# Kernel optimization log

Hardware: AMD Instinct MI355X
Metric: run time of the kernel (lower is better)

## Reference

```python
import jax, jax.numpy as jnp
import numpy as np

F_, OF, OW, L, H, NH = 40, 8, 24, 3, 128, 4
G = F_ // OF  # 5 groups
B, T = 32, 512


def setup_inputs() -> dict:
    key = jax.random.key(0)
    ks = jax.random.split(key, 17)
    s = 0.08
    rn = lambda k, shape: jax.random.normal(k, shape, jnp.float32) * s
    return {
        "x": jax.random.normal(ks[0], (B, F_, T), jnp.float32),
        # per-feature stacked 3-layer LSTM params (PyTorch gate order i,f,g,o)
        "w_ih0": rn(ks[1], (F_, 4 * H, 1)),
        "w_ih12": rn(ks[2], (L - 1, F_, 4 * H, H)),
        "w_hh": rn(ks[3], (L, F_, 4 * H, H)),
        "b_ih": rn(ks[4], (L, F_, 4 * H)),
        "b_hh": rn(ks[5], (L, F_, 4 * H)),
        # per-group MHA params
        "g_wqkv": rn(ks[6], (G, 3 * H, H)),
        "g_bqkv": rn(ks[7], (G, 3 * H)),
        "g_wo": rn(ks[8], (G, H, H)),
        "g_bo": rn(ks[9], (G, H)),
        # final MHA params
        "f_wqkv": rn(ks[10], (3 * H, H)),
        "f_bqkv": rn(ks[11], (3 * H,)),
        "f_wo": rn(ks[12], (H, H)),
        "f_bo": rn(ks[13], (H,)),
        # output FC
        "fc_w": rn(ks[14], (OF * OW, H)),
        "fc_b": rn(ks[15], (OF * OW,)),
    }


def _lstm_layer(xw, whh, bhh):
    # xw: [F,B,T,4H] precomputed input projections; scan over time
    h0 = jnp.zeros(xw.shape[:2] + (H,), xw.dtype)
    def step(carry, xt):
        h, c = carry
        gates = xt + jnp.einsum('fbh,fgh->fbg', h, whh) + bhh[:, None, :]
        i, f, g, o = jnp.split(gates, 4, axis=-1)
        c = jax.nn.sigmoid(f) * c + jax.nn.sigmoid(i) * jnp.tanh(g)
        h = jax.nn.sigmoid(o) * jnp.tanh(c)
        return (h, c), h
    (hT, _), hs = jax.lax.scan(step, (h0, h0), jnp.moveaxis(xw, 2, 0))
    return jnp.moveaxis(hs, 0, 2), hT  # seq [F,B,T,H], last [F,B,H]


def _mha(q, k, v, wqkv, bqkv, wo, bo):
    wq, wk, wv = jnp.split(wqkv, 3, axis=0)
    bq, bk, bv = jnp.split(bqkv, 3, axis=0)
    hd = H // NH
    def proj(t, w, b):
        p = t @ w.T + b
        return p.reshape(t.shape[:-1] + (NH, hd)).swapaxes(-3, -2)  # [..,NH,S,hd]
    qh, kh, vh = proj(q, wq, bq), proj(k, wk, bk), proj(v, wv, bv)
    scores = jnp.einsum('bnqd,bnkd->bnqk', qh, kh) / np.float32(np.sqrt(hd))
    attn = jax.nn.softmax(scores, axis=-1)
    out = jnp.einsum('bnqk,bnkd->bnqd', attn, vh).swapaxes(-3, -2).reshape(q.shape)
    return out @ wo.T + bo


def reference(x, w_ih0, w_ih12, w_hh, b_ih, b_hh, g_wqkv, g_bqkv, g_wo, g_bo,
              f_wqkv, f_bqkv, f_wo, f_bo, fc_w, fc_b):
    bsz = x.shape[0]
    h_seq = jnp.transpose(x, (1, 0, 2))[..., None]  # [F,B,T,1]
    h_last = None
    for l in range(L):  # 3 stacked LSTM layers, all 40 feature-LSTMs batched
        wih = w_ih0 if l == 0 else w_ih12[l - 1]
        xw = jnp.einsum('fbti,fgi->fbtg', h_seq, wih) + b_ih[l][:, None, None, :]
        h_seq, h_last = _lstm_layer(xw, w_hh[l], b_hh[l])
    features = jnp.transpose(h_last, (1, 0, 2))  # [B,F,H]
    groups = features.reshape(bsz, G, OF, H).swapaxes(0, 1)  # [G,B,OF,H]
    gattn = jax.vmap(lambda g, w, b, wo, bo: _mha(g, g, g, w, b, wo, bo))(
        groups, g_wqkv, g_bqkv, g_wo, g_bo)  # [G,B,OF,H]
    pooled = gattn.mean(axis=2).swapaxes(0, 1)  # [B,G,H]
    fin = _mha(pooled, pooled, pooled, f_wqkv, f_bqkv, f_wo, f_bo)  # [B,G,H]
    emb = fin[:, 0, :]  # target_coin_index = 0
    return (emb @ fc_w.T + fc_b).reshape(bsz, OF, OW)
```

## Files before the change

### kernel.cpp

```cpp
#include <hip/hip_runtime.h>
#include <cstdint>
#include <cstddef>


#define NFEAT 40
#define TDIM  512

typedef __bf16 bf16x8 __attribute__((ext_vector_type(8)));
typedef float floatx4 __attribute__((ext_vector_type(4)));
typedef float floatx2 __attribute__((ext_vector_type(2)));
typedef int   intx4   __attribute__((ext_vector_type(4)));
typedef unsigned short u16;

#if __has_builtin(__builtin_amdgcn_exp2f)
#define EXP2F __builtin_amdgcn_exp2f
#else
#define EXP2F exp2f
#endif
#if __has_builtin(__builtin_amdgcn_rcpf)
#define RCPF __builtin_amdgcn_rcpf
#else
#define RCPF(x) (1.f / (x))
#endif

#define MF(a, b, c) __builtin_amdgcn_mfma_f32_16x16x32_bf16( \
    __builtin_bit_cast(bf16x8, (a)), __builtin_bit_cast(bf16x8, (b)), (c), 0, 0, 0)

#define NEG_LOG2E -1.44269504f

__device__ __forceinline__ float bf2f(u16 s) {
  union { unsigned u; float f; } v; v.u = ((unsigned)s) << 16; return v.f;
}
__device__ __forceinline__ unsigned f2bf(float f) {
  union { float f; unsigned u; } v; v.f = f;
  unsigned u = v.u + 0x7fffu + ((v.u >> 16) & 1u);
  return (u >> 16);
}

#define RING_FSTRIDE 1048576
#define RING_TSTRIDE 4096
#define RING_MASK    255

__global__ void prep_kernel(const float* __restrict__ w_ih12,
                            const float* __restrict__ w_hh,
                            const float* __restrict__ b_ih,
                            const float* __restrict__ b_hh,
                            u16* __restrict__ Whh,
                            u16* __restrict__ Wih,
                            float* __restrict__ biasAll,
                            int* __restrict__ flags)
{
  const int N_hh4 = 3 * NFEAT * 512 * 128 / 4;
  const int N_ih4 = 2 * NFEAT * 512 * 128 / 4;
  const int NB    = 3 * NFEAT * 512;
  const int NF    = 384;
  const int total = N_hh4 + N_ih4 + NB + NF;
  for (int idx = blockIdx.x * blockDim.x + threadIdx.x; idx < total;
       idx += gridDim.x * blockDim.x) {
    if (idx < N_hh4 + N_ih4) {
      const bool ih = (idx >= N_hh4);
      const int i4 = (ih ? idx - N_hh4 : idx) * 4;
      const float4 v = *(const float4*)((ih ? w_ih12 : w_hh) + i4);
      uint2 p;
      p.x = (f2bf(v.y * NEG_LOG2E) << 16) | f2bf(v.x * NEG_LOG2E);
      p.y = (f2bf(v.w * NEG_LOG2E) << 16) | f2bf(v.z * NEG_LOG2E);
      *(uint2*)((ih ? Wih : Whh) + i4) = p;
    } else if (idx < N_hh4 + N_ih4 + NB) {
      int i = idx - N_hh4 - N_ih4;
      biasAll[i] = (b_ih[i] + b_hh[i]) * NEG_LOG2E;
    } else {
      flags[idx - N_hh4 - N_ih4 - NB] = 0;
    }
  }
}

template <int LAYER>
__device__ __forceinline__ void lstm_body(
    const u16* __restrict__ Wh, const u16* __restrict__ Wx,
    const float* __restrict__ bias,
    const float* __restrict__ xin, const float* __restrict__ w0,
    const u16* __restrict__ ringIn, u16* __restrict__ ringOut,
    u16* __restrict__ hlast,
    int* __restrict__ flagIn,
    int* __restrict__ flagOut,
    int* __restrict__ flagConsIn,
    int* __restrict__ flagConsOut,
    int f, int half, u16* __restrict__ Abase)
{
  constexpr bool IS_L0   = (LAYER == 0);
  constexpr bool IS_LAST = (LAYER == 2);

  const int tid  = threadIdx.x;
  const int wave = tid >> 6;
  const int lane = tid & 63;
  const int m15  = lane & 15;
  const int q    = lane >> 4;
  const int kb   = q * 8;
  const int wq4  = wave * 16 + q * 4;

#define ALDS(P, M, K) (Abase + ((P) * 16 + (M)) * 136 + (K))

  intx4 whf[4][4];
  const size_t wbase = (size_t)f * 512 * 128;
#pragma unroll
  for (int g = 0; g < 4; ++g)
#pragma unroll
    for (int kt = 0; kt < 4; ++kt)
      whf[g][kt] = *(const intx4*)(Wh + wbase +
          (size_t)(g * 128 + wave * 16 + m15) * 128 + kt * 32 + kb);

  intx4 wxf[4][4];
  if constexpr (!IS_L0) {
#pragma unroll
    for (int g = 0; g < 4; ++g)
#pragma unroll
      for (int kt = 0; kt < 4; ++kt)
        wxf[g][kt] = *(const intx4*)(Wx + wbase +
            (size_t)(g * 128 + wave * 16 + m15) * 128 + kt * 32 + kb);
  }

  floatx4 bv[4], w0v[4];
#pragma unroll
  for (int g = 0; g < 4; ++g) {
    bv[g] = *(const floatx4*)(bias + f * 512 + g * 128 + wq4);
    if constexpr (IS_L0) {
      floatx4 wv = *(const floatx4*)(w0 + f * 512 + g * 128 + wq4);
      w0v[g] = wv * NEG_LOG2E;
    }
  }

  for (int idx = tid; idx < 2 * 16 * 136; idx += 512) Abase[idx] = 0;

  if constexpr (LAYER >= 1) {
    if (tid == 0) {
      while (__hip_atomic_load(flagIn, __ATOMIC_RELAXED,
                               __HIP_MEMORY_SCOPE_AGENT) < 19)
        __builtin_amdgcn_s_sleep(2);
      __threadfence();
    }
  }
  __syncthreads();

  const u16* xbase = (LAYER >= 1)
      ? ringIn + (size_t)f * RING_FSTRIDE + (half * 16 + m15) * 128 + kb
      : nullptr;
  const float* xsbase = IS_L0
      ? xin + ((size_t)(half * 16 + m15) * NFEAT + f) * 512
      : nullptr;

  floatx4 accx0[4], accx1[4];
  intx4 xf0[4], xf1[4];
  float xsc[2] = {0.f, 0.f};

  if constexpr (!IS_L0) {
    intx4 p0[4];
#pragma unroll
    for (int kt = 0; kt < 4; ++kt) p0[kt]  = *(const intx4*)(xbase + kt * 32);
#pragma unroll
    for (int kt = 0; kt < 4; ++kt)
      xf0[kt] = *(const intx4*)(xbase + 1 * RING_TSTRIDE + kt * 32);
#pragma unroll
    for (int kt = 0; kt < 4; ++kt)
      xf1[kt] = *(const intx4*)(xbase + 2 * RING_TSTRIDE + kt * 32);
#pragma unroll
    for (int g = 0; g < 4; ++g) {
      floatx4 a = bv[g];
#pragma unroll
      for (int kt = 0; kt < 4; ++kt) a = MF(wxf[g][kt], p0[kt], a);
      accx0[g] = a;
    }
  } else {
    const float x0 = xsbase[0];
    xsc[0] = xsbase[1];
    xsc[1] = xsbase[2];
#pragma unroll
    for (int g = 0; g < 4; ++g) accx0[g] = bv[g] + w0v[g] * x0;
  }

  float creg[4] = {0.f, 0.f, 0.f, 0.f};
  u16* hb_ring = (LAYER <= 1)
      ? ringOut + (size_t)f * RING_FSTRIDE + (half * 16 + m15) * 128 + wq4
      : nullptr;
  uint2 hdef;

#define LSTM_STEP(PC, ACC_C, ACC_N, XF_C, T)                                   \
  {                                                                            \
                                            \
    if (((T) & 15) == 0 && (T) > 0) {                                          \
      if (tid == 0) {                                                          \
        if constexpr (LAYER >= 1) {                                            \
          int tgt = (T) + 19; if (tgt > 512) tgt = 512;                        \
          while (__hip_atomic_load(flagIn, __ATOMIC_RELAXED,                   \
                                   __HIP_MEMORY_SCOPE_AGENT) < tgt)            \
            __builtin_amdgcn_s_sleep(2);                                       \
        }                                                                      \
        if constexpr (LAYER <= 1) {                                            \
                               \
          while (__hip_atomic_load(flagConsIn, __ATOMIC_RELAXED,               \
                                   __HIP_MEMORY_SCOPE_AGENT) < (T) - 290)      \
            __builtin_amdgcn_s_sleep(2);                                       \
        }                                                                      \
        __threadfence();       \
        if constexpr (LAYER <= 1)                                              \
          __hip_atomic_store(flagOut, (T) - 2, __ATOMIC_RELAXED,               \
                             __HIP_MEMORY_SCOPE_AGENT);                        \
        if constexpr (LAYER >= 1)                                              \
          __hip_atomic_store(flagConsOut, (T), __ATOMIC_RELAXED,               \
                             __HIP_MEMORY_SCOPE_AGENT);                        \
      }                                                                        \
      if constexpr (LAYER >= 1) __syncthreads();                               \
    }                                                                          \
                                 \
    if constexpr (!IS_LAST) {                                                  \
      if ((T) > 0)                                                             \
        *(uint2*)(hb_ring + (size_t)(((T) - 1) & RING_MASK) * RING_TSTRIDE) =  \
            hdef;                                                              \
    }                                                                          \
                                            \
    intx4 xn0, xn1, xn2, xn3;                                                  \
    float xns = 0.f;                                                           \
    {                                                                          \
      const int tl = ((T) + 3 < TDIM) ? (T) + 3 : TDIM - 1;                    \
      if constexpr (!IS_L0) {                                                  \
        const u16* xp = xbase + (size_t)(tl & RING_MASK) * RING_TSTRIDE;       \
        xn0 = *(const intx4*)(xp);                                             \
        xn1 = *(const intx4*)(xp + 32);                                        \
        xn2 = *(const intx4*)(xp + 64);                                        \
        xn3 = *(const intx4*)(xp + 96);                                        \
      } else {                                                                 \
        xns = xsbase[tl];                                                      \
      }                                                                        \
    }                                                                          \
                                                     \
    intx4 hf0 = *(const intx4*)ALDS(PC, m15, kb);                              \
    intx4 hf1 = *(const intx4*)ALDS(PC, m15, 32 + kb);                         \
    intx4 hf2 = *(const intx4*)ALDS(PC, m15, 64 + kb);                         \
    intx4 hf3 = *(const intx4*)ALDS(PC, m15, 96 + kb);                         \
                                                   \
    floatx4 ac0 = MF(whf[0][0], hf0, ACC_C[0]);                                \
    floatx4 ac1 = MF(whf[1][0], hf0, ACC_C[1]);                                \
    floatx4 ac2 = MF(whf[2][0], hf0, ACC_C[2]);                                \
    floatx4 ac3 = MF(whf[3][0], hf0, ACC_C[3]);                                \
    ac0 = MF(whf[0][1], hf1, ac0); ac1 = MF(whf[1][1], hf1, ac1);              \
    ac2 = MF(whf[2][1], hf1, ac2); ac3 = MF(whf[3][1], hf1, ac3);              \
    ac0 = MF(whf[0][2], hf2, ac0); ac1 = MF(whf[1][2], hf2, ac1);              \
    ac2 = MF(whf[2][2], hf2, ac2); ac3 = MF(whf[3][2], hf2, ac3);              \
    ac0 = MF(whf[0][3], hf3, ac0); ac1 = MF(whf[1][3], hf3, ac1);              \
    ac2 = MF(whf[2][3], hf3, ac2); ac3 = MF(whf[3][3], hf3, ac3);              \
             \
    if constexpr (!IS_L0) {                                                    \
      floatx4 n0 = bv[0], n1 = bv[1], n2 = bv[2], n3 = bv[3];                  \
      n0 = MF(wxf[0][0], XF_C[0], n0); n1 = MF(wxf[1][0], XF_C[0], n1);        \
      n2 = MF(wxf[2][0], XF_C[0], n2); n3 = MF(wxf[3][0], XF_C[0], n3);        \
      n0 = MF(wxf[0][1], XF_C[1], n0); n1 = MF(wxf[1][1], XF_C[1], n1);        \
      n2 = MF(wxf[2][1], XF_C[1], n2); n3 = MF(wxf[3][1], XF_C[1], n3);        \
      n0 = MF(wxf[0][2], XF_C[2], n0); n1 = MF(wxf[1][2], XF_C[2], n1);        \
      n2 = MF(wxf[2][2], XF_C[2], n2); n3 = MF(wxf[3][2], XF_C[2], n3);        \
      n0 = MF(wxf[0][3], XF_C[3], n0); n1 = MF(wxf[1][3], XF_C[3], n1);        \
      n2 = MF(wxf[2][3], XF_C[3], n2); n3 = MF(wxf[3][3], XF_C[3], n3);        \
      ACC_N[0] = n0; ACC_N[1] = n1; ACC_N[2] = n2; ACC_N[3] = n3;              \
      XF_C[0] = xn0; XF_C[1] = xn1; XF_C[2] = xn2; XF_C[3] = xn3;              \
    } else {                                                                   \
      const float xn = xsc[PC];                                                \
      ACC_N[0] = bv[0] + w0v[0] * xn; ACC_N[1] = bv[1] + w0v[1] * xn;          \
      ACC_N[2] = bv[2] + w0v[2] * xn; ACC_N[3] = bv[3] + w0v[3] * xn;          \
      xsc[PC] = xns;                                                           \
    }                                                                          \
                 \
    unsigned hlo, hhi;                                                         \
    {                                                                          \
      float hv[4];                                                             \
      _Pragma("unroll")                                                        \
      for (int r = 0; r < 4; ++r) {                                            \
        const float Ei = EXP2F(ac0[r]);                                        \
        const float Ef = EXP2F(ac1[r]);                                        \
        const float Eg = EXP2F(2.f * ac2[r]);                                  \
        const float Eo = EXP2F(ac3[r]);                                        \
        const float Pp = (1.f + Ei) * (1.f + Eg);                              \
        const float Qq = 1.f + Ef;                                             \
        const float c  = (creg[r] * Pp + Qq * (1.f - Eg)) * RCPF(Qq * Pp);     \
        creg[r] = c;                                                           \
        const float Ec = EXP2F(-2.88539008f * c);                              \
        hv[r] = (1.f - Ec) * RCPF((1.f + Ec) * (1.f + Eo));                    \
      }                                                                        \
      hlo = (f2bf(hv[1]) << 16) | f2bf(hv[0]);                                 \
      hhi = (f2bf(hv[3]) << 16) | f2bf(hv[2]);                                 \
    }                                                                          \
    uint2 hp; hp.x = hlo; hp.y = hhi;                                          \
    *(uint2*)ALDS((PC) ^ 1, m15, wq4) = hp;                                    \
    hdef = hp;                                                                 \
    __syncthreads();                                                           \
  }

#pragma unroll 1
  for (int t = 0; t < TDIM; t += 2) {
    LSTM_STEP(0, accx0, accx1, xf0, t);
    LSTM_STEP(1, accx1, accx0, xf1, t + 1);
  }
#undef LSTM_STEP
#undef ALDS

  if constexpr (!IS_LAST) {
    *(uint2*)(hb_ring + (size_t)(511 & RING_MASK) * RING_TSTRIDE) = hdef;
    __syncthreads();
    if (tid == 0) {
      __threadfence();
      __hip_atomic_store(flagOut, 512, __ATOMIC_RELAXED,
                         __HIP_MEMORY_SCOPE_AGENT);
    }
  } else {
    *(uint2*)(hlast + ((size_t)f * 32 + half * 16 + m15) * 128 + wq4) = hdef;
  }
}

__global__ __launch_bounds__(512, 2) void lstm_fused(
    const u16* __restrict__ Whh, const u16* __restrict__ Wih,
    const float* __restrict__ biasAll,
    const float* __restrict__ xin, const float* __restrict__ w0,
    u16* __restrict__ ring0, u16* __restrict__ ring1,
    u16* __restrict__ hlast, int* __restrict__ flags)
{
  __shared__ __align__(16) u16 A[2 * 16 * 136];
  const int layer = blockIdx.x / 80;
  const int bx    = blockIdx.x % 80;
  const int f = bx >> 1, half = bx & 1;
  const size_t LSL = (size_t)NFEAT * 512 * 128;

  if (layer == 0) {
    lstm_body<0>(Whh, nullptr, biasAll, xin, w0,
                 nullptr, ring0, nullptr,
                 nullptr, flags + bx, flags + 160 + bx, nullptr,
                 f, half, A);
  } else if (layer == 1) {
    lstm_body<1>(Whh + LSL, Wih, biasAll + NFEAT * 512, nullptr, nullptr,
                 ring0, ring1, nullptr,
                 flags + bx, flags + 80 + bx, flags + 240 + bx,
                 flags + 160 + bx, f, half, A);
  } else {
    lstm_body<2>(Whh + 2 * LSL, Wih + LSL, biasAll + 2 * NFEAT * 512,
                 nullptr, nullptr, ring1, nullptr, hlast,
                 flags + 80 + bx, nullptr, nullptr, flags + 240 + bx,
                 f, half, A);
  }
}

__global__ void gattn_kernel(const u16* __restrict__ hlast,
                             const float* __restrict__ g_wqkv,
                             const float* __restrict__ g_bqkv,
                             const float* __restrict__ g_wo,
                             const float* __restrict__ g_bo,
                             float* __restrict__ pooled)
{
  const int tid = threadIdx.x;
  const int g = blockIdx.x >> 5;
  const int b = blockIdx.x & 31;

  __shared__ float feat[8][128];
  __shared__ float qkv[8][384];
  __shared__ float sc[4][8][8];
  __shared__ float colsum[4][8];
  __shared__ float poolin[128];

  for (int idx = tid; idx < 8 * 128; idx += 128) {
    int of = idx >> 7, j = idx & 127;
    int f = g * 8 + of;
    feat[of][j] = bf2f(hlast[((size_t)f * 32 + b) * 128 + j]);
  }
  __syncthreads();
  for (int idx = tid; idx < 8 * 384; idx += 128) {
    int of = idx / 384, r = idx - of * 384;
    const float* wr = g_wqkv + ((size_t)g * 384 + r) * 128;
    float s = 0.f;
    for (int j = 0; j < 128; ++j) s += feat[of][j] * wr[j];
    qkv[of][r] = s + g_bqkv[g * 384 + r];
  }
  __syncthreads();
  for (int idx = tid; idx < 256; idx += 128) {
    int n = idx >> 6, qp = (idx >> 3) & 7, kp = idx & 7;
    float s = 0.f;
    for (int d = 0; d < 32; ++d)
      s += qkv[qp][n * 32 + d] * qkv[kp][128 + n * 32 + d];
    sc[n][qp][kp] = s * 0.17677669529663687f;
  }
  __syncthreads();
  if (tid < 32) {
    int n = tid >> 3, qp = tid & 7;
    float mx = -1e30f;
    for (int kp = 0; kp < 8; ++kp) mx = fmaxf(mx, sc[n][qp][kp]);
    float e[8], sum = 0.f;
    for (int kp = 0; kp < 8; ++kp) { e[kp] = __expf(sc[n][qp][kp] - mx); sum += e[kp]; }
    float inv = 1.f / sum;
    for (int kp = 0; kp < 8; ++kp) sc[n][qp][kp] = e[kp] * inv;
  }
  __syncthreads();
  if (tid < 32) {
    int n = tid >> 3, kp = tid & 7;
    float s = 0.f;
    for (int qp = 0; qp < 8; ++qp) s += sc[n][qp][kp];
    colsum[n][kp] = s;
  }
  __syncthreads();
  {
    int n = tid >> 5;
    float s = 0.f;
    for (int kp = 0; kp < 8; ++kp) s += colsum[n][kp] * qkv[kp][256 + tid];
    poolin[tid] = s;
  }
  __syncthreads();
  {
    const float* wr = g_wo + ((size_t)g * 128 + tid) * 128;
    float s = 0.f;
    for (int i = 0; i < 128; ++i) s += poolin[i] * wr[i];
    pooled[((size_t)b * 5 + g) * 128 + tid] = s * 0.125f + g_bo[g * 128 + tid];
  }
}

__global__ void final_kernel(const float* __restrict__ pooled,
                             const float* __restrict__ f_wqkv,
                             const float* __restrict__ f_bqkv,
                             const float* __restrict__ f_wo,
                             const float* __restrict__ f_bo,
                             const float* __restrict__ fc_w,
                             const float* __restrict__ fc_b,
                             float* __restrict__ out)
{
  const int tid = threadIdx.x;
  const int b = blockIdx.x;

  __shared__ float P[5][128];
  __shared__ float q0[128];
  __shared__ float kbuf[5][128];
  __shared__ float vbuf[5][128];
  __shared__ float attn[4][5];
  __shared__ float ao[128];
  __shared__ float fin[128];

  for (int idx = tid; idx < 640; idx += 192) {
    int g = idx >> 7, j = idx & 127;
    P[g][j] = pooled[((size_t)b * 5 + g) * 128 + j];
  }
  __syncthreads();
  for (int idx = tid; idx < 1408; idx += 192) {
    int kind, pos, r;
    if (idx < 128)       { kind = 0; pos = 0;                 r = idx; }
    else if (idx < 768)  { kind = 1; pos = (idx - 128) >> 7;  r = (idx - 128) & 127; }
    else                 { kind = 2; pos = (idx - 768) >> 7;  r = (idx - 768) & 127; }
    const int wrow = kind * 128 + r;
    const float* wr = f_wqkv + (size_t)wrow * 128;
    const float* src = P[kind == 0 ? 0 : pos];
    float s = 0.f;
    for (int j = 0; j < 128; ++j) s += src[j] * wr[j];
    s += f_bqkv[wrow];
    if (kind == 0) q0[r] = s;
    else if (kind == 1) kbuf[pos][r] = s;
    else vbuf[pos][r] = s;
  }
  __syncthreads();
  if (tid < 20) {
    int n = tid / 5, kp = tid - n * 5;
    float s = 0.f;
    for (int d = 0; d < 32; ++d) s += q0[n * 32 + d] * kbuf[kp][n * 32 + d];
    attn[n][kp] = s * 0.17677669529663687f;
  }
  __syncthreads();
  if (tid < 4) {
    float mx = -1e30f;
    for (int kp = 0; kp < 5; ++kp) mx = fmaxf(mx, attn[tid][kp]);
    float sum = 0.f;
    for (int kp = 0; kp < 5; ++kp) { float e = __expf(attn[tid][kp] - mx); attn[tid][kp] = e; sum += e; }
    float inv = 1.f / sum;
    for (int kp = 0; kp < 5; ++kp) attn[tid][kp] *= inv;
  }
  __syncthreads();
  if (tid < 128) {
    int n = tid >> 5;
    float s = 0.f;
    for (int kp = 0; kp < 5; ++kp) s += attn[n][kp] * vbuf[kp][tid];
    ao[tid] = s;
  }
  __syncthreads();
  if (tid < 128) {
    const float* wr = f_wo + (size_t)tid * 128;
    float s = 0.f;
    for (int i = 0; i < 128; ++i) s += ao[i] * wr[i];
    fin[tid] = s + f_bo[tid];
  }
  __syncthreads();
  {
    const float* wr = fc_w + (size_t)tid * 128;
    float s = 0.f;
    for (int j = 0; j < 128; ++j) s += fin[j] * wr[j];
    out[(size_t)b * 192 + tid] = s + fc_b[tid];
  }
}

extern "C" void kernel_launch(void* const* d_in, const int* in_sizes, int n_in,
                              void* d_out, int out_size, void* d_ws, size_t ws_size,
                              hipStream_t stream)
{
  const float* x      = (const float*)d_in[0];
  const float* w_ih0  = (const float*)d_in[1];
  const float* w_ih12 = (const float*)d_in[2];
  const float* w_hh   = (const float*)d_in[3];
  const float* b_ih   = (const float*)d_in[4];
  const float* b_hh   = (const float*)d_in[5];
  const float* g_wqkv = (const float*)d_in[6];
  const float* g_bqkv = (const float*)d_in[7];
  const float* g_wo   = (const float*)d_in[8];
  const float* g_bo   = (const float*)d_in[9];
  const float* f_wqkv = (const float*)d_in[10];
  const float* f_bqkv = (const float*)d_in[11];
  const float* f_wo   = (const float*)d_in[12];
  const float* f_bo   = (const float*)d_in[13];
  const float* fc_w   = (const float*)d_in[14];
  const float* fc_b   = (const float*)d_in[15];

  const size_t N_hh = (size_t)3 * NFEAT * 512 * 128;
  const size_t N_ih = (size_t)2 * NFEAT * 512 * 128;
  const size_t NB   = (size_t)3 * NFEAT * 512;
  const size_t RSZ  = (size_t)NFEAT * 256 * 4096;

  u16* Whh       = (u16*)d_ws;
  u16* Wih       = Whh + N_hh;
  float* biasAll = (float*)(Wih + N_ih);
  u16* ring0     = (u16*)(biasAll + NB);
  u16* ring1     = ring0 + RSZ;
  u16* hlast     = ring1 + RSZ;
  int* flags     = (int*)(hlast + (size_t)NFEAT * 32 * 128);
  float* pooled  = (float*)(flags + 384);

  prep_kernel<<<4096, 256, 0, stream>>>(w_ih12, w_hh, b_ih, b_hh,
                                        Whh, Wih, biasAll, flags);

  lstm_fused<<<240, 512, 0, stream>>>(Whh, Wih, biasAll, x, w_ih0,
                                      ring0, ring1, hlast, flags);

  gattn_kernel<<<160, 128, 0, stream>>>(hlast, g_wqkv, g_bqkv, g_wo, g_bo, pooled);
  final_kernel<<<32, 192, 0, stream>>>(pooled, f_wqkv, f_bqkv, f_wo, f_bo,
                                       fc_w, fc_b, (float*)d_out);
}
```

Before: 977.8 us.

## Replace threadfence with agent-scope atomic ring accesses and tighten consumer lag

```diff
diff --git a/kernel.cpp b/kernel.cpp
--- a/kernel.cpp
+++ b/kernel.cpp
@@ -8,9 +8,9 @@
 
 typedef __bf16 bf16x8 __attribute__((ext_vector_type(8)));
 typedef float floatx4 __attribute__((ext_vector_type(4)));
-typedef float floatx2 __attribute__((ext_vector_type(2)));
 typedef int   intx4   __attribute__((ext_vector_type(4)));
 typedef unsigned short u16;
+typedef unsigned long long u64;
 
 #if __has_builtin(__builtin_amdgcn_exp2f)
 #define EXP2F __builtin_amdgcn_exp2f
@@ -35,6 +35,19 @@
   union { float f; unsigned u; } v; v.f = f;
   unsigned u = v.u + 0x7fffu + ((v.u >> 16) & 1u);
   return (u >> 16);
+}
+
+__device__ __forceinline__ void st_ring8(u16* p, uint2 v) {
+  u64 q = ((u64)v.y << 32) | (u64)v.x;
+  __hip_atomic_store((u64*)p, q, __ATOMIC_RELAXED, __HIP_MEMORY_SCOPE_AGENT);
+}
+__device__ __forceinline__ intx4 ld_ring16(const u16* p) {
+  union { u64 q[2]; intx4 v; } u;
+  u.q[0] = __hip_atomic_load((const u64*)p, __ATOMIC_RELAXED,
+                             __HIP_MEMORY_SCOPE_AGENT);
+  u.q[1] = __hip_atomic_load((const u64*)(p + 4), __ATOMIC_RELAXED,
+                             __HIP_MEMORY_SCOPE_AGENT);
+  return u.v;
 }
 
 #define RING_FSTRIDE 1048576
@@ -136,7 +149,6 @@
       while (__hip_atomic_load(flagIn, __ATOMIC_RELAXED,
                                __HIP_MEMORY_SCOPE_AGENT) < 19)
         __builtin_amdgcn_s_sleep(2);
-      __threadfence();
     }
   }
   __syncthreads();
@@ -155,13 +167,13 @@
   if constexpr (!IS_L0) {
     intx4 p0[4];
 #pragma unroll
-    for (int kt = 0; kt < 4; ++kt) p0[kt]  = *(const intx4*)(xbase + kt * 32);
+    for (int kt = 0; kt < 4; ++kt) p0[kt]  = ld_ring16(xbase + kt * 32);
 #pragma unroll
     for (int kt = 0; kt < 4; ++kt)
-      xf0[kt] = *(const intx4*)(xbase + 1 * RING_TSTRIDE + kt * 32);
+      xf0[kt] = ld_ring16(xbase + 1 * RING_TSTRIDE + kt * 32);
 #pragma unroll
     for (int kt = 0; kt < 4; ++kt)
-      xf1[kt] = *(const intx4*)(xbase + 2 * RING_TSTRIDE + kt * 32);
+      xf1[kt] = ld_ring16(xbase + 2 * RING_TSTRIDE + kt * 32);
 #pragma unroll
     for (int g = 0; g < 4; ++g) {
       floatx4 a = bv[g];
@@ -185,7 +197,7 @@
 
 #define LSTM_STEP(PC, ACC_C, ACC_N, XF_C, T)                                   \
   {                                                                            \
-                                            \
+      \
     if (((T) & 15) == 0 && (T) > 0) {                                          \
       if (tid == 0) {                                                          \
         if constexpr (LAYER >= 1) {                                            \
@@ -195,12 +207,14 @@
             __builtin_amdgcn_s_sleep(2);                                       \
         }                                                                      \
         if constexpr (LAYER <= 1) {                                            \
-                               \
+                          \
           while (__hip_atomic_load(flagConsIn, __ATOMIC_RELAXED,               \
-                                   __HIP_MEMORY_SCOPE_AGENT) < (T) - 290)      \
+                                   __HIP_MEMORY_SCOPE_AGENT) < (T) - 240)      \
             __builtin_amdgcn_s_sleep(2);                                       \
         }                                                                      \
-        __threadfence();       \
+      }                                                                        \
+      __syncthreads();       \
+      if (tid == 0) {                                                          \
         if constexpr (LAYER <= 1)                                              \
           __hip_atomic_store(flagOut, (T) - 2, __ATOMIC_RELAXED,               \
                              __HIP_MEMORY_SCOPE_AGENT);                        \
@@ -208,13 +222,12 @@
           __hip_atomic_store(flagConsOut, (T), __ATOMIC_RELAXED,               \
                              __HIP_MEMORY_SCOPE_AGENT);                        \
       }                                                                        \
-      if constexpr (LAYER >= 1) __syncthreads();                               \
     }                                                                          \
-                                 \
+                           \
     if constexpr (!IS_LAST) {                                                  \
       if ((T) > 0)                                                             \
-        *(uint2*)(hb_ring + (size_t)(((T) - 1) & RING_MASK) * RING_TSTRIDE) =  \
-            hdef;                                                              \
+        st_ring8(hb_ring + (size_t)(((T) - 1) & RING_MASK) * RING_TSTRIDE,     \
+                 hdef);                                                        \
     }                                                                          \
                                             \
     intx4 xn0, xn1, xn2, xn3;                                                  \
@@ -223,10 +236,10 @@
       const int tl = ((T) + 3 < TDIM) ? (T) + 3 : TDIM - 1;                    \
       if constexpr (!IS_L0) {                                                  \
         const u16* xp = xbase + (size_t)(tl & RING_MASK) * RING_TSTRIDE;       \
-        xn0 = *(const intx4*)(xp);                                             \
-        xn1 = *(const intx4*)(xp + 32);                                        \
-        xn2 = *(const intx4*)(xp + 64);                                        \
-        xn3 = *(const intx4*)(xp + 96);                                        \
+        xn0 = ld_ring16(xp);                                                   \
+        xn1 = ld_ring16(xp + 32);                                              \
+        xn2 = ld_ring16(xp + 64);                                              \
+        xn3 = ld_ring16(xp + 96);                                              \
       } else {                                                                 \
         xns = xsbase[tl];                                                      \
       }                                                                        \
@@ -301,13 +314,11 @@
 #undef ALDS
 
   if constexpr (!IS_LAST) {
-    *(uint2*)(hb_ring + (size_t)(511 & RING_MASK) * RING_TSTRIDE) = hdef;
+    st_ring8(hb_ring + (size_t)(511 & RING_MASK) * RING_TSTRIDE, hdef);
     __syncthreads();
-    if (tid == 0) {
-      __threadfence();
+    if (tid == 0)
       __hip_atomic_store(flagOut, 512, __ATOMIC_RELAXED,
                          __HIP_MEMORY_SCOPE_AGENT);
-    }
   } else {
     *(uint2*)(hlast + ((size_t)f * 32 + half * 16 + m15) * 128 + wq4) = hdef;
   }
```

Result: slower. 1.448 ms (+48.1%).
